# Performance work log

Hardware: AMD Instinct MI355X
Metric: run time of the kernel (lower is better)

## Reference

```python
import jax, jax.numpy as jnp
import numpy as np

NEG_LARGE = -2.0**32 + 1.0


def setup_inputs() -> dict:
    key = jax.random.key(0)
    ks = jax.random.split(key, 8)
    B, L, D = 2048, 200, 64  # D = embedding_dim, features are 2D wide
    H1, H2 = 80, 40
    queries = jax.random.normal(ks[0], (B, 2 * D), dtype=jnp.float32)
    user_behaviors = jax.random.normal(ks[1], (B, L, 2 * D), dtype=jnp.float32)
    masks = jax.random.randint(ks[2], (B, L), 0, 2, dtype=jnp.int32)
    s = 1.0 / np.sqrt(8 * D)
    w1 = jax.random.uniform(ks[3], (8 * D, H1), minval=-s, maxval=s, dtype=jnp.float32)
    b1 = jnp.zeros((H1,), jnp.float32)
    s2 = 1.0 / np.sqrt(H1)
    w2 = jax.random.uniform(ks[4], (H1, H2), minval=-s2, maxval=s2, dtype=jnp.float32)
    b2 = jnp.zeros((H2,), jnp.float32)
    s3 = 1.0 / np.sqrt(H2)
    w3 = jax.random.uniform(ks[5], (H2, 1), minval=-s3, maxval=s3, dtype=jnp.float32)
    b3 = jnp.zeros((1,), jnp.float32)
    return {"queries": queries, "user_behaviors": user_behaviors, "masks": masks,
            "w1": w1, "b1": b1, "w2": w2, "b2": b2, "w3": w3, "b3": b3}


def reference(queries, user_behaviors, masks, w1, b1, w2, b2, w3, b3):
    B, L, twoD = user_behaviors.shape
    q = jnp.broadcast_to(queries[:, None, :], (B, L, twoD))  # (B, L, 2D)
    feats = jnp.concatenate([q, user_behaviors, q - user_behaviors,
                             q * user_behaviors], axis=-1)  # (B, L, 8D)
    h = jax.nn.sigmoid(jnp.einsum('blf,fh->blh', feats, w1) + b1)
    h = jax.nn.sigmoid(jnp.einsum('blh,hk->blk', h, w2) + b2)
    scores = jnp.einsum('blk,ko->blo', h, w3) + b3  # (B, L, 1)
    valid = (masks != 0)[:, :, None]
    scores = jnp.where(valid, scores, NEG_LARGE)
    attn = jax.nn.softmax(scores, axis=1)  # (B, L, 1)
    return jnp.sum(attn * user_behaviors, axis=1)  # (B, 2D)
```

## Files before the change

### kernel.cpp

```cpp
#include <hip/hip_runtime.h>
#include <cstddef>


#define L_   200
#define D2_  128

typedef __attribute__((ext_vector_type(8))) short bf16x8;
typedef __attribute__((ext_vector_type(4))) float f32x4;
typedef __attribute__((ext_vector_type(4))) unsigned int u32x4;

union U8 { u32x4 u; bf16x8 b; };

__device__ __forceinline__ float sigmoidf_(float x) { return 1.0f / (1.0f + __expf(-x)); }

__device__ __forceinline__ unsigned int f2bf_(float x) {
  unsigned int u = __float_as_uint(x);
  return (u + 0x7fffu + ((u >> 16) & 1u)) >> 16;
}
__device__ __forceinline__ unsigned int pk2_(float a, float b) {
  return f2bf_(a) | (f2bf_(b) << 16);
}

extern "C" __global__ void __launch_bounds__(128)
din_setup_kernel(const float* __restrict__ queries,
                 const float* __restrict__ w1,
                 const float* __restrict__ b1,
                 const float* __restrict__ w2,
                 float* __restrict__ qt,
                 float* __restrict__ wbc,
                 float* __restrict__ wd,
                 u32x4* __restrict__ w2a,
                 u32x4* __restrict__ w2b)
{
  const int bb = blockIdx.x;
  const int t  = threadIdx.x;

  if (bb < 8) {
    for (int s = bb * 160 + t; s < bb * 160 + 160; s += 128) {
      int nn = s & 15, kg = (s >> 4) & 3, g = s >> 6;
      int kc = g / 5, nt = g - kc * 5;
      int h = nt * 16 + nn, k0 = kc * 32 + kg * 8;
      #pragma unroll
      for (int j = 0; j < 8; ++j) {
        int k = k0 + j;
        wbc[s * 8 + j] = w1[(128 + k) * 80 + h] - w1[(256 + k) * 80 + h];
        wd [s * 8 + j] = w1[(384 + k) * 80 + h];
      }
    }
  } else if (bb == 8) {
    for (int s = t; s < 384; s += 128) {
      int nn = s & 15, g = s >> 4, nt2 = g >> 3, kg = g & 7;
      int j = nt2 * 16 + nn, k0 = kg * 8;
      u32x4 v = { 0u, 0u, 0u, 0u };
      if (j < 40) {
        float e0 = w2[(k0 + 0) * 40 + j], e1 = w2[(k0 + 1) * 40 + j];
        float e2 = w2[(k0 + 2) * 40 + j], e3 = w2[(k0 + 3) * 40 + j];
        float e4 = w2[(k0 + 4) * 40 + j], e5 = w2[(k0 + 5) * 40 + j];
        float e6 = w2[(k0 + 6) * 40 + j], e7 = w2[(k0 + 7) * 40 + j];
        v = (u32x4){ pk2_(e0, e1), pk2_(e2, e3), pk2_(e4, e5), pk2_(e6, e7) };
      }
      w2a[s] = v;
    }
    for (int s = t; s < 96; s += 128) {
      int nn = s & 15, g = s >> 4, nt2 = g >> 1, kgt = g & 1;
      int j = nt2 * 16 + nn, k0 = 64 + kgt * 8;
      u32x4 v = { 0u, 0u, 0u, 0u };
      if (j < 40) {
        float e0 = w2[(k0 + 0) * 40 + j], e1 = w2[(k0 + 1) * 40 + j];
        float e2 = w2[(k0 + 2) * 40 + j], e3 = w2[(k0 + 3) * 40 + j];
        float e4 = w2[(k0 + 4) * 40 + j], e5 = w2[(k0 + 5) * 40 + j];
        float e6 = w2[(k0 + 6) * 40 + j], e7 = w2[(k0 + 7) * 40 + j];
        v = (u32x4){ pk2_(e0, e1), pk2_(e2, e3), pk2_(e4, e5), pk2_(e6, e7) };
      }
      w2b[s] = v;
    }
  } else {
    const int b = bb - 9;
    __shared__ float qs[128];
    if (t < 128) qs[t] = queries[(size_t)b * D2_ + t];
    __syncthreads();
    if (t < 80) {
      float acc = b1[t];
      #pragma unroll 4
      for (int k = 0; k < 128; ++k)
        acc += qs[k] * (w1[k * 80 + t] + w1[(256 + k) * 80 + t]);
      qt[(size_t)b * 80 + t] = acc;
    }
  }
}

extern "C" __global__ void __launch_bounds__(256, 4)
din_attn_kernel(const float* __restrict__ queries,
                const float* __restrict__ ub,
                const int*   __restrict__ masks,
                const float* __restrict__ b2,
                const float* __restrict__ w3,
                const float* __restrict__ qt,
                const float* __restrict__ wbc,
                const float* __restrict__ wd,
                const u32x4* __restrict__ w2a,
                const u32x4* __restrict__ w2b,
                float* __restrict__ out)
{
  __shared__ __align__(16) char  pool[33280];
  __shared__ __align__(16) float wsum_s[1088];
  __shared__ __align__(16) float qt_s[80];
  __shared__ __align__(16) float b2_s[48];
  __shared__ __align__(16) float w3_s[48];
  __shared__ __align__(16) float scores_s[208];
  __shared__ float red_s[8];

  const int b    = blockIdx.x;
  const int t    = threadIdx.x;
  const int wave = t >> 6;
  const int lane = t & 63;
  const int n16  = lane & 15;
  const int rg   = lane >> 4;

  const float* ubbase = ub + (size_t)b * (L_ * D2_);
  const float* qrow   = queries + (size_t)b * D2_;

  if (t < 80) qt_s[t] = qt[(size_t)b * 80 + t];
  if (t < 48) {
    b2_s[t] = (t < 40) ? b2[t] : 0.0f;
    w3_s[t] = (t < 40) ? w3[t] : 0.0f;
  }

  {
    u32x4* dst = (u32x4*)pool;
    const float4* wbc4 = (const float4*)wbc;
    const float4* wd4  = (const float4*)wd;
    #pragma unroll
    for (int i = 0; i < 5; ++i) {
      int s = i * 256 + t;
      int kg = (s >> 4) & 3, g = s >> 6;
      int kc = g / 5;
      int k0 = kc * 32 + kg * 8;
      float4 c0 = wbc4[2 * s], c1 = wbc4[2 * s + 1];
      float4 d0 = wd4 [2 * s], d1 = wd4 [2 * s + 1];
      float4 q0 = *(const float4*)(qrow + k0);
      float4 q1 = *(const float4*)(qrow + k0 + 4);
      dst[s] = (u32x4){ pk2_(c0.x + q0.x * d0.x, c0.y + q0.y * d0.y),
                        pk2_(c0.z + q0.z * d0.z, c0.w + q0.w * d0.w),
                        pk2_(c1.x + q1.x * d1.x, c1.y + q1.y * d1.y),
                        pk2_(c1.z + q1.z * d1.z, c1.w + q1.w * d1.w) };
    }
  }
  __syncthreads();

  f32x4 acc[4][5];
  #pragma unroll
  for (int i = 0; i < 4; ++i)
    #pragma unroll
    for (int nt = 0; nt < 5; ++nt) acc[i][nt] = (f32x4){0.f, 0.f, 0.f, 0.f};

  const bf16x8* Bf = (const bf16x8*)pool;

  for (int kc = 0; kc < 4; ++kc) {
    bf16x8 bvv[5];
    #pragma unroll
    for (int nt = 0; nt < 5; ++nt) bvv[nt] = Bf[(kc * 5 + nt) * 64 + lane];
    #pragma unroll
    for (int i = 0; i < 4; ++i) {
      int mt = wave + i * 4;
      if (mt < 13) {
        int row = mt * 16 + n16;
        float4 u0 = make_float4(0.f, 0.f, 0.f, 0.f);
        float4 u1 = make_float4(0.f, 0.f, 0.f, 0.f);
        if (row < L_) {
          const float4* src = (const float4*)(ubbase + (size_t)row * D2_ + kc * 32 + rg * 8);
          u0 = src[0]; u1 = src[1];
        }
        U8 av;
        av.u = (u32x4){ pk2_(u0.x, u0.y), pk2_(u0.z, u0.w),
                        pk2_(u1.x, u1.y), pk2_(u1.z, u1.w) };
        #pragma unroll
        for (int nt = 0; nt < 5; ++nt)
          acc[i][nt] = __builtin_amdgcn_mfma_f32_16x16x32_bf16(av.b, bvv[nt], acc[i][nt], 0, 0, 0);
      }
    }
  }
  __syncthreads();

  {
    unsigned short* hv = (unsigned short*)pool;
    #pragma unroll
    for (int i = 0; i < 4; ++i) {
      int mt = wave + i * 4;
      if (mt < 13) {
        #pragma unroll
        for (int nt = 0; nt < 5; ++nt) {
          int h = nt * 16 + n16;
          float qtv = qt_s[h];
          int kg = h >> 3;
          int slotbase = (kg < 8) ? (mt * 8 + kg) : (1664 + mt * 2 + (kg - 8));
          #pragma unroll
          for (int r = 0; r < 4; ++r) {
            float x = acc[i][nt][r] + qtv;
            hv[(slotbase * 16 + rg * 4 + r) * 8 + (h & 7)] =
                (unsigned short)f2bf_(sigmoidf_(x));
          }
        }
      }
    }
  }

  {
    const bf16x8* hvf  = (const bf16x8*)pool;
    const bf16x8* w2af = (const bf16x8*)w2a;
    const bf16x8* w2bf = (const bf16x8*)w2b;
    #pragma unroll
    for (int i = 0; i < 4; ++i) {
      int mt = wave + i * 4;
      if (mt < 13) {
        f32x4 acc2[3];
        #pragma unroll
        for (int n2 = 0; n2 < 3; ++n2) acc2[n2] = (f32x4){0.f, 0.f, 0.f, 0.f};

        #pragma unroll
        for (int ks = 0; ks < 2; ++ks) {
          bf16x8 av = hvf[(mt * 8 + ks * 4 + rg) * 16 + n16];
          #pragma unroll
          for (int n2 = 0; n2 < 3; ++n2) {
            bf16x8 bv = w2af[(n2 * 8 + ks * 4 + rg) * 16 + n16];
            acc2[n2] = __builtin_amdgcn_mfma_f32_16x16x32_bf16(av, bv, acc2[n2], 0, 0, 0);
          }
        }
        {
          bf16x8 av = (bf16x8){0, 0, 0, 0, 0, 0, 0, 0};
          if (lane < 32) av = hvf[(1664 + mt * 2 + rg) * 16 + n16];
          #pragma unroll
          for (int n2 = 0; n2 < 3; ++n2) {
            bf16x8 bv = (bf16x8){0, 0, 0, 0, 0, 0, 0, 0};
            if (lane < 32) bv = w2bf[(n2 * 2 + rg) * 16 + n16];
            acc2[n2] = __builtin_amdgcn_mfma_f32_16x16x32_bf16(av, bv, acc2[n2], 0, 0, 0);
          }
        }

        #pragma unroll
        for (int r = 0; r < 4; ++r) {
          float s = 0.0f;
          #pragma unroll
          for (int n2 = 0; n2 < 3; ++n2) {
            int j = n2 * 16 + n16;
            s += sigmoidf_(acc2[n2][r] + b2_s[j]) * w3_s[j];
          }
          s += __shfl_xor(s, 1, 64);
          s += __shfl_xor(s, 2, 64);
          s += __shfl_xor(s, 4, 64);
          s += __shfl_xor(s, 8, 64);
          int l = mt * 16 + rg * 4 + r;
          if (n16 == 0 && l < L_) scores_s[l] = s;
        }
      }
    }
  }
  __syncthreads();

  float sval = -INFINITY;
  if (t < L_) {
    int mv = masks[(size_t)b * L_ + t];
    sval = mv ? scores_s[t] : -4294967295.0f;
  }
  float m = sval;
  #pragma unroll
  for (int o = 32; o > 0; o >>= 1) m = fmaxf(m, __shfl_xor(m, o, 64));
  if (lane == 0) red_s[wave] = m;
  __syncthreads();
  m = fmaxf(fmaxf(red_s[0], red_s[1]), fmaxf(red_s[2], red_s[3]));
  float e = (t < L_) ? __expf(sval - m) : 0.0f;
  float ssum = e;
  #pragma unroll
  for (int o = 32; o > 0; o >>= 1) ssum += __shfl_xor(ssum, o, 64);
  if (lane == 0) red_s[4 + wave] = ssum;
  __syncthreads();
  ssum = red_s[4] + red_s[5] + red_s[6] + red_s[7];
  float attn = e / ssum;
  __syncthreads();
  if (t < L_) scores_s[t] = attn;
  __syncthreads();

  {
    const float4* ub4base = (const float4*)ubbase;
    int d4 = t & 31;
    int lg = t >> 5;
    float4 o = make_float4(0.f, 0.f, 0.f, 0.f);
    #pragma unroll 5
    for (int l = lg; l < L_; l += 8) {
      float w = scores_s[l];
      float4 v = ub4base[l * 32 + d4];
      o.x += w * v.x; o.y += w * v.y; o.z += w * v.z; o.w += w * v.w;
    }
    *(float4*)(wsum_s + lg * 136 + d4 * 4) = o;
    __syncthreads();
    if (t < 128) {
      float s = 0.0f;
      #pragma unroll
      for (int g = 0; g < 8; ++g) s += wsum_s[g * 136 + t];
      out[(size_t)b * 128 + t] = s;
    }
  }
}

extern "C" void kernel_launch(void* const* d_in, const int* in_sizes, int n_in,
                              void* d_out, int out_size, void* d_ws, size_t ws_size,
                              hipStream_t stream) {
  const float* queries = (const float*)d_in[0];
  const float* ub      = (const float*)d_in[1];
  const int*   masks   = (const int*)d_in[2];
  const float* w1      = (const float*)d_in[3];
  const float* b1      = (const float*)d_in[4];
  const float* w2      = (const float*)d_in[5];
  const float* b2      = (const float*)d_in[6];
  const float* w3      = (const float*)d_in[7];
  float* out = (float*)d_out;

  const int B = in_sizes[0] / D2_;

  char*  ws  = (char*)d_ws;
  float* qt  = (float*)ws;
  float* wbc = (float*)(ws + (size_t)B * 320);
  float* wd  = (float*)(ws + (size_t)B * 320 + 40960);
  u32x4* w2a = (u32x4*)(ws + (size_t)B * 320 + 81920);
  u32x4* w2b = (u32x4*)(ws + (size_t)B * 320 + 88064);

  din_setup_kernel<<<B + 9, 128, 0, stream>>>(queries, w1, b1, w2, qt, wbc, wd, w2a, w2b);
  din_attn_kernel<<<B, 256, 0, stream>>>(queries, ub, masks, b2, w3,
                                         qt, wbc, wd, w2a, w2b, out);
}
```

Measured before the change: 358.1 us.

## Software-pipeline behavior loads in the layer-1 MFMA loop and use hardware bf16 conversion

The layer-1 GEMM is restructured into a fully unrolled, double-buffered sequence. The first behavior-row loads are issued before the shared-memory weight setup, so global latency overlaps that setup and each MFMA step. Out-of-range rows are clamped rather than branched around, so some waves now do wasted MFMA work on padded tiles. Float-to-bf16 packing uses the v_cvt_pk_bf16_f32 instruction, and occupancy is lowered to 3 blocks per SM to make room for the extra registers. The mask load is hoisted to the kernel start, one redundant barrier is removed, and the final weighted-sum loop is fully unrolled.

```diff
diff --git a/kernel.cpp b/kernel.cpp
--- a/kernel.cpp
+++ b/kernel.cpp
@@ -19,6 +19,11 @@
 }
 __device__ __forceinline__ unsigned int pk2_(float a, float b) {
   return f2bf_(a) | (f2bf_(b) << 16);
+}
+__device__ __forceinline__ unsigned int pk2f_(float a, float b) {
+  unsigned int r;
+  asm("v_cvt_pk_bf16_f32 %0, %1, %2" : "=v"(r) : "v"(a), "v"(b));
+  return r;
 }
 
 extern "C" __global__ void __launch_bounds__(128)
@@ -89,7 +94,7 @@
   }
 }
 
-extern "C" __global__ void __launch_bounds__(256, 4)
+extern "C" __global__ void __launch_bounds__(256, 3)
 din_attn_kernel(const float* __restrict__ queries,
                 const float* __restrict__ ub,
                 const int*   __restrict__ masks,
@@ -120,11 +125,65 @@
   const float* ubbase = ub + (size_t)b * (L_ * D2_);
   const float* qrow   = queries + (size_t)b * D2_;
 
+  int mv_early = 1;
+  if (t < L_) mv_early = masks[(size_t)b * L_ + t];
   if (t < 80) qt_s[t] = qt[(size_t)b * 80 + t];
   if (t < 48) {
     b2_s[t] = (t < 40) ? b2[t] : 0.0f;
     w3_s[t] = (t < 40) ? w3[t] : 0.0f;
   }
+
+  const float* pa[4];
+  #pragma unroll
+  for (int i = 0; i < 4; ++i) {
+    int row = (wave + i * 4) * 16 + n16;
+    int rc  = (row < L_) ? row : (L_ - 1);
+    pa[i] = ubbase + (size_t)rc * D2_ + rg * 8;
+  }
+
+  f32x4 acc[4][5];
+  #pragma unroll
+  for (int i = 0; i < 4; ++i)
+    #pragma unroll
+    for (int nt = 0; nt < 5; ++nt) acc[i][nt] = (f32x4){0.f, 0.f, 0.f, 0.f};
+
+  const bf16x8* Bf = (const bf16x8*)pool;
+  bf16x8 bvv[5];
+  float4 A0, A1, B0, B1;
+
+#define LOADP(X0, X1, P) do { \
+    const float4* s_ = (const float4*)(pa[(P) & 3] + ((P) >> 2) * 32); \
+    X0 = s_[0]; X1 = s_[1]; \
+  } while (0)
+
+#define LOADB(KC) do { \
+    bvv[0] = Bf[((KC) * 5 + 0) * 64 + lane]; \
+    bvv[1] = Bf[((KC) * 5 + 1) * 64 + lane]; \
+    bvv[2] = Bf[((KC) * 5 + 2) * 64 + lane]; \
+    bvv[3] = Bf[((KC) * 5 + 3) * 64 + lane]; \
+    bvv[4] = Bf[((KC) * 5 + 4) * 64 + lane]; \
+  } while (0)
+
+#define COMPP(X0, X1, P) do { \
+    U8 av_; \
+    av_.u = (u32x4){ pk2f_(X0.x, X0.y), pk2f_(X0.z, X0.w), \
+                     pk2f_(X1.x, X1.y), pk2f_(X1.z, X1.w) }; \
+    const int i_ = (P) & 3; \
+    acc[i_][0] = __builtin_amdgcn_mfma_f32_16x16x32_bf16(av_.b, bvv[0], acc[i_][0], 0, 0, 0); \
+    acc[i_][1] = __builtin_amdgcn_mfma_f32_16x16x32_bf16(av_.b, bvv[1], acc[i_][1], 0, 0, 0); \
+    acc[i_][2] = __builtin_amdgcn_mfma_f32_16x16x32_bf16(av_.b, bvv[2], acc[i_][2], 0, 0, 0); \
+    acc[i_][3] = __builtin_amdgcn_mfma_f32_16x16x32_bf16(av_.b, bvv[3], acc[i_][3], 0, 0, 0); \
+    acc[i_][4] = __builtin_amdgcn_mfma_f32_16x16x32_bf16(av_.b, bvv[4], acc[i_][4], 0, 0, 0); \
+  } while (0)
+
+#define STEP(X0, X1, P) do { \
+    COMPP(X0, X1, P); \
+    if ((P) + 2 < 16) LOADP(X0, X1, (P) + 2); \
+    if (((P) & 3) == 3 && (P) < 12) LOADB(((P) >> 2) + 1); \
+  } while (0)
+
+  LOADP(A0, A1, 0);
+  LOADP(B0, B1, 1);
 
   {
     u32x4* dst = (u32x4*)pool;
@@ -140,46 +199,24 @@
       float4 d0 = wd4 [2 * s], d1 = wd4 [2 * s + 1];
       float4 q0 = *(const float4*)(qrow + k0);
       float4 q1 = *(const float4*)(qrow + k0 + 4);
-      dst[s] = (u32x4){ pk2_(c0.x + q0.x * d0.x, c0.y + q0.y * d0.y),
-                        pk2_(c0.z + q0.z * d0.z, c0.w + q0.w * d0.w),
-                        pk2_(c1.x + q1.x * d1.x, c1.y + q1.y * d1.y),
-                        pk2_(c1.z + q1.z * d1.z, c1.w + q1.w * d1.w) };
-    }
-  }
-  __syncthreads();
-
-  f32x4 acc[4][5];
-  #pragma unroll
-  for (int i = 0; i < 4; ++i)
-    #pragma unroll
-    for (int nt = 0; nt < 5; ++nt) acc[i][nt] = (f32x4){0.f, 0.f, 0.f, 0.f};
-
-  const bf16x8* Bf = (const bf16x8*)pool;
-
-  for (int kc = 0; kc < 4; ++kc) {
-    bf16x8 bvv[5];
-    #pragma unroll
-    for (int nt = 0; nt < 5; ++nt) bvv[nt] = Bf[(kc * 5 + nt) * 64 + lane];
-    #pragma unroll
-    for (int i = 0; i < 4; ++i) {
-      int mt = wave + i * 4;
-      if (mt < 13) {
-        int row = mt * 16 + n16;
-        float4 u0 = make_float4(0.f, 0.f, 0.f, 0.f);
-        float4 u1 = make_float4(0.f, 0.f, 0.f, 0.f);
-        if (row < L_) {
-          const float4* src = (const float4*)(ubbase + (size_t)row * D2_ + kc * 32 + rg * 8);
-          u0 = src[0]; u1 = src[1];
-        }
-        U8 av;
-        av.u = (u32x4){ pk2_(u0.x, u0.y), pk2_(u0.z, u0.w),
-                        pk2_(u1.x, u1.y), pk2_(u1.z, u1.w) };
-        #pragma unroll
-        for (int nt = 0; nt < 5; ++nt)
-          acc[i][nt] = __builtin_amdgcn_mfma_f32_16x16x32_bf16(av.b, bvv[nt], acc[i][nt], 0, 0, 0);
-      }
-    }
-  }
+      dst[s] = (u32x4){ pk2f_(c0.x + q0.x * d0.x, c0.y + q0.y * d0.y),
+                        pk2f_(c0.z + q0.z * d0.z, c0.w + q0.w * d0.w),
+                        pk2f_(c1.x + q1.x * d1.x, c1.y + q1.y * d1.y),
+                        pk2f_(c1.z + q1.z * d1.z, c1.w + q1.w * d1.w) };
+    }
+  }
+  __syncthreads();
+
+  LOADB(0);
+  STEP(A0, A1, 0);  STEP(B0, B1, 1);
+  STEP(A0, A1, 2);  STEP(B0, B1, 3);
+  STEP(A0, A1, 4);  STEP(B0, B1, 5);
+  STEP(A0, A1, 6);  STEP(B0, B1, 7);
+  STEP(A0, A1, 8);  STEP(B0, B1, 9);
+  STEP(A0, A1, 10); STEP(B0, B1, 11);
+  STEP(A0, A1, 12); STEP(B0, B1, 13);
+  STEP(A0, A1, 14); STEP(B0, B1, 15);
+
   __syncthreads();
 
   {
@@ -258,10 +295,7 @@
   __syncthreads();
 
   float sval = -INFINITY;
-  if (t < L_) {
-    int mv = masks[(size_t)b * L_ + t];
-    sval = mv ? scores_s[t] : -4294967295.0f;
-  }
+  if (t < L_) sval = mv_early ? scores_s[t] : -4294967295.0f;
   float m = sval;
   #pragma unroll
   for (int o = 32; o > 0; o >>= 1) m = fmaxf(m, __shfl_xor(m, o, 64));
@@ -275,9 +309,7 @@
   if (lane == 0) red_s[4 + wave] = ssum;
   __syncthreads();
   ssum = red_s[4] + red_s[5] + red_s[6] + red_s[7];
-  float attn = e / ssum;
-  __syncthreads();
-  if (t < L_) scores_s[t] = attn;
+  if (t < L_) scores_s[t] = e / ssum;
   __syncthreads();
 
   {
@@ -285,7 +317,7 @@
     int d4 = t & 31;
     int lg = t >> 5;
     float4 o = make_float4(0.f, 0.f, 0.f, 0.f);
-    #pragma unroll 5
+    #pragma unroll
     for (int l = lg; l < L_; l += 8) {
       float w = scores_s[l];
       float4 v = ub4base[l * 32 + d4];
@@ -300,6 +332,11 @@
       out[(size_t)b * 128 + t] = s;
     }
   }
+
+#undef LOADP
+#undef LOADB
+#undef COMPP
+#undef STEP
 }
 
 extern "C" void kernel_launch(void* const* d_in, const int* in_sizes, int n_in,
```

After: 382.3 us. +6.8%, slower.

## Prefetch behavior rows into registers and hoist B fragments out of MFMA loop

Applied to the files above, without the earlier changes.

The first-layer MFMA loop now software-pipelines global loads of the user-behavior rows, issuing the first two k-chunks before the weight-prep phase and double-buffering the remaining chunks in registers. All 20 B fragments are loaded from LDS into registers once, up front. Other changes: the packing uses the hardware v_cvt_pk_bf16_f32 instruction, the mask load moves to kernel start, one redundant barrier is dropped, and the weighted-sum loop is fully unrolled. Register pressure rises sharply, which may lower occupancy. Out-of-range rows are clamped to row 199 rather than zeroed, and those rows' results are discarded later.

```diff
diff --git a/kernel.cpp b/kernel.cpp
--- a/kernel.cpp
+++ b/kernel.cpp
@@ -19,6 +19,11 @@
 }
 __device__ __forceinline__ unsigned int pk2_(float a, float b) {
   return f2bf_(a) | (f2bf_(b) << 16);
+}
+__device__ __forceinline__ unsigned int pk2f_(float a, float b) {
+  unsigned int r;
+  asm("v_cvt_pk_bf16_f32 %0, %1, %2" : "=v"(r) : "v"(a), "v"(b));
+  return r;
 }
 
 extern "C" __global__ void __launch_bounds__(128)
@@ -120,11 +125,35 @@
   const float* ubbase = ub + (size_t)b * (L_ * D2_);
   const float* qrow   = queries + (size_t)b * D2_;
 
+  int mv_early = 1;
+  if (t < L_) mv_early = masks[(size_t)b * L_ + t];
   if (t < 80) qt_s[t] = qt[(size_t)b * 80 + t];
   if (t < 48) {
     b2_s[t] = (t < 40) ? b2[t] : 0.0f;
     w3_s[t] = (t < 40) ? w3[t] : 0.0f;
   }
+
+  const float* pa[4];
+  #pragma unroll
+  for (int i = 0; i < 4; ++i) {
+    int row = (wave + i * 4) * 16 + n16;
+    int rc  = (row < L_) ? row : (L_ - 1);
+    pa[i] = ubbase + (size_t)rc * D2_ + rg * 8;
+  }
+
+  float4 ca[4], cb[4], da[4], db[4];
+  #pragma unroll
+  for (int i = 0; i < 4; ++i)
+    if (i < 3 || wave == 0) {
+      const float4* s0 = (const float4*)(pa[i]);
+      ca[i] = s0[0]; cb[i] = s0[1];
+    }
+  #pragma unroll
+  for (int i = 0; i < 4; ++i)
+    if (i < 3 || wave == 0) {
+      const float4* s1 = (const float4*)(pa[i] + 32);
+      da[i] = s1[0]; db[i] = s1[1];
+    }
 
   {
     u32x4* dst = (u32x4*)pool;
@@ -140,12 +169,18 @@
       float4 d0 = wd4 [2 * s], d1 = wd4 [2 * s + 1];
       float4 q0 = *(const float4*)(qrow + k0);
       float4 q1 = *(const float4*)(qrow + k0 + 4);
-      dst[s] = (u32x4){ pk2_(c0.x + q0.x * d0.x, c0.y + q0.y * d0.y),
-                        pk2_(c0.z + q0.z * d0.z, c0.w + q0.w * d0.w),
-                        pk2_(c1.x + q1.x * d1.x, c1.y + q1.y * d1.y),
-                        pk2_(c1.z + q1.z * d1.z, c1.w + q1.w * d1.w) };
-    }
-  }
+      dst[s] = (u32x4){ pk2f_(c0.x + q0.x * d0.x, c0.y + q0.y * d0.y),
+                        pk2f_(c0.z + q0.z * d0.z, c0.w + q0.w * d0.w),
+                        pk2f_(c1.x + q1.x * d1.x, c1.y + q1.y * d1.y),
+                        pk2f_(c1.z + q1.z * d1.z, c1.w + q1.w * d1.w) };
+    }
+  }
+  __syncthreads();
+
+  const bf16x8* Bf = (const bf16x8*)pool;
+  bf16x8 bf[20];
+  #pragma unroll
+  for (int x = 0; x < 20; ++x) bf[x] = Bf[x * 64 + lane];
   __syncthreads();
 
   f32x4 acc[4][5];
@@ -154,33 +189,28 @@
     #pragma unroll
     for (int nt = 0; nt < 5; ++nt) acc[i][nt] = (f32x4){0.f, 0.f, 0.f, 0.f};
 
-  const bf16x8* Bf = (const bf16x8*)pool;
-
+  #pragma unroll
   for (int kc = 0; kc < 4; ++kc) {
-    bf16x8 bvv[5];
-    #pragma unroll
-    for (int nt = 0; nt < 5; ++nt) bvv[nt] = Bf[(kc * 5 + nt) * 64 + lane];
     #pragma unroll
     for (int i = 0; i < 4; ++i) {
-      int mt = wave + i * 4;
-      if (mt < 13) {
-        int row = mt * 16 + n16;
-        float4 u0 = make_float4(0.f, 0.f, 0.f, 0.f);
-        float4 u1 = make_float4(0.f, 0.f, 0.f, 0.f);
-        if (row < L_) {
-          const float4* src = (const float4*)(ubbase + (size_t)row * D2_ + kc * 32 + rg * 8);
-          u0 = src[0]; u1 = src[1];
-        }
+      if (i < 3 || wave == 0) {
+        float4 x0 = (kc & 1) ? da[i] : ca[i];
+        float4 x1 = (kc & 1) ? db[i] : cb[i];
         U8 av;
-        av.u = (u32x4){ pk2_(u0.x, u0.y), pk2_(u0.z, u0.w),
-                        pk2_(u1.x, u1.y), pk2_(u1.z, u1.w) };
+        av.u = (u32x4){ pk2f_(x0.x, x0.y), pk2f_(x0.z, x0.w),
+                        pk2f_(x1.x, x1.y), pk2f_(x1.z, x1.w) };
+        if (kc < 2) {
+          const float4* s2 = (const float4*)(pa[i] + (kc + 2) * 32);
+          if (kc & 1) { da[i] = s2[0]; db[i] = s2[1]; }
+          else        { ca[i] = s2[0]; cb[i] = s2[1]; }
+        }
         #pragma unroll
         for (int nt = 0; nt < 5; ++nt)
-          acc[i][nt] = __builtin_amdgcn_mfma_f32_16x16x32_bf16(av.b, bvv[nt], acc[i][nt], 0, 0, 0);
-      }
-    }
-  }
-  __syncthreads();
+          acc[i][nt] = __builtin_amdgcn_mfma_f32_16x16x32_bf16(av.b, bf[kc * 5 + nt],
+                                                               acc[i][nt], 0, 0, 0);
+      }
+    }
+  }
 
   {
     unsigned short* hv = (unsigned short*)pool;
@@ -258,10 +288,7 @@
   __syncthreads();
 
   float sval = -INFINITY;
-  if (t < L_) {
-    int mv = masks[(size_t)b * L_ + t];
-    sval = mv ? scores_s[t] : -4294967295.0f;
-  }
+  if (t < L_) sval = mv_early ? scores_s[t] : -4294967295.0f;
   float m = sval;
   #pragma unroll
   for (int o = 32; o > 0; o >>= 1) m = fmaxf(m, __shfl_xor(m, o, 64));
@@ -275,9 +302,7 @@
   if (lane == 0) red_s[4 + wave] = ssum;
   __syncthreads();
   ssum = red_s[4] + red_s[5] + red_s[6] + red_s[7];
-  float attn = e / ssum;
-  __syncthreads();
-  if (t < L_) scores_s[t] = attn;
+  if (t < L_) scores_s[t] = e / ssum;
   __syncthreads();
 
   {
@@ -285,7 +310,7 @@
     int d4 = t & 31;
     int lg = t >> 5;
     float4 o = make_float4(0.f, 0.f, 0.f, 0.f);
-    #pragma unroll 5
+    #pragma unroll
     for (int l = lg; l < L_; l += 8) {
       float w = scores_s[l];
       float4 v = ub4base[l * 32 + d4];
```

Result: slower. 481.2 us (+34.4%).

## Split attention kernel into two-block score kernel plus softmax/weighted-sum kernel

Applied to the files above, without the earlier changes.

The fused per-batch attention kernel is split in two. A scores kernel runs two blocks per batch row, each covering part of the 13 row tiles, with per-wave LDS scratch for the hidden layer and smaller shared memory, and writes scores to a workspace buffer. A second kernel then does the masked softmax and the weighted sum over user behaviors. The bf16 packing switches to the hardware v_cvt_pk_bf16_f32 instruction. The aim is more parallelism and occupancy, at the cost of an extra launch, an extra workspace round trip, and reading user_behaviors twice across kernels. The old fused kernel stays as a fallback when the workspace is too small.

```diff
diff --git a/kernel.cpp b/kernel.cpp
--- a/kernel.cpp
+++ b/kernel.cpp
@@ -19,6 +19,11 @@
 }
 __device__ __forceinline__ unsigned int pk2_(float a, float b) {
   return f2bf_(a) | (f2bf_(b) << 16);
+}
+__device__ __forceinline__ unsigned int pk2f_(float a, float b) {
+  unsigned int r;
+  asm("v_cvt_pk_bf16_f32 %0, %1, %2" : "=v"(r) : "v"(a), "v"(b));
+  return r;
 }
 
 extern "C" __global__ void __launch_bounds__(128)
@@ -90,32 +95,34 @@
 }
 
 extern "C" __global__ void __launch_bounds__(256, 4)
-din_attn_kernel(const float* __restrict__ queries,
-                const float* __restrict__ ub,
-                const int*   __restrict__ masks,
-                const float* __restrict__ b2,
-                const float* __restrict__ w3,
-                const float* __restrict__ qt,
-                const float* __restrict__ wbc,
-                const float* __restrict__ wd,
-                const u32x4* __restrict__ w2a,
-                const u32x4* __restrict__ w2b,
-                float* __restrict__ out)
+din_scores_kernel(const float* __restrict__ queries,
+                  const float* __restrict__ ub,
+                  const float* __restrict__ b2,
+                  const float* __restrict__ w3,
+                  const float* __restrict__ qt,
+                  const float* __restrict__ wbc,
+                  const float* __restrict__ wd,
+                  const u32x4* __restrict__ w2a,
+                  const u32x4* __restrict__ w2b,
+                  float* __restrict__ scores_ws)
 {
-  __shared__ __align__(16) char  pool[33280];
-  __shared__ __align__(16) float wsum_s[1088];
+  __shared__ __align__(16) char  pool[20480];
+  __shared__ __align__(16) char  scratch[10240];
   __shared__ __align__(16) float qt_s[80];
   __shared__ __align__(16) float b2_s[48];
   __shared__ __align__(16) float w3_s[48];
-  __shared__ __align__(16) float scores_s[208];
-  __shared__ float red_s[8];
-
-  const int b    = blockIdx.x;
-  const int t    = threadIdx.x;
-  const int wave = t >> 6;
-  const int lane = t & 63;
-  const int n16  = lane & 15;
-  const int rg   = lane >> 4;
+
+  const int bc    = blockIdx.x;
+  const int b     = bc >> 1;
+  const int chunk = bc & 1;
+  const int t     = threadIdx.x;
+  const int wave  = t >> 6;
+  const int lane  = t & 63;
+  const int n16   = lane & 15;
+  const int rg    = lane >> 4;
+
+  const int st  = chunk ? (wave < 2 ? 7 + wave * 2 : 9 + wave) : wave * 2;
+  const int cnt = chunk ? (wave < 2 ? 2 : 1) : (wave < 3 ? 2 : 1);
 
   const float* ubbase = ub + (size_t)b * (L_ * D2_);
   const float* qrow   = queries + (size_t)b * D2_;
@@ -140,10 +147,232 @@
       float4 d0 = wd4 [2 * s], d1 = wd4 [2 * s + 1];
       float4 q0 = *(const float4*)(qrow + k0);
       float4 q1 = *(const float4*)(qrow + k0 + 4);
-      dst[s] = (u32x4){ pk2_(c0.x + q0.x * d0.x, c0.y + q0.y * d0.y),
-                        pk2_(c0.z + q0.z * d0.z, c0.w + q0.w * d0.w),
-                        pk2_(c1.x + q1.x * d1.x, c1.y + q1.y * d1.y),
-                        pk2_(c1.z + q1.z * d1.z, c1.w + q1.w * d1.w) };
+      dst[s] = (u32x4){ pk2f_(c0.x + q0.x * d0.x, c0.y + q0.y * d0.y),
+                        pk2f_(c0.z + q0.z * d0.z, c0.w + q0.w * d0.w),
+                        pk2f_(c1.x + q1.x * d1.x, c1.y + q1.y * d1.y),
+                        pk2f_(c1.z + q1.z * d1.z, c1.w + q1.w * d1.w) };
+    }
+  }
+  __syncthreads();
+
+  const float* pa[2];
+  #pragma unroll
+  for (int i = 0; i < 2; ++i) {
+    int row = (st + i) * 16 + n16;
+    int rc  = (row < L_) ? row : (L_ - 1);
+    pa[i] = ubbase + (size_t)rc * D2_ + rg * 8;
+  }
+
+  f32x4 acc[2][5];
+  #pragma unroll
+  for (int i = 0; i < 2; ++i)
+    #pragma unroll
+    for (int nt = 0; nt < 5; ++nt) acc[i][nt] = (f32x4){0.f, 0.f, 0.f, 0.f};
+
+  const bf16x8* Bf = (const bf16x8*)pool;
+  for (int kc = 0; kc < 4; ++kc) {
+    U8 av[2];
+    #pragma unroll
+    for (int i = 0; i < 2; ++i) {
+      if (i < cnt) {
+        const float4* src = (const float4*)(pa[i] + kc * 32);
+        float4 u0 = src[0], u1 = src[1];
+        av[i].u = (u32x4){ pk2f_(u0.x, u0.y), pk2f_(u0.z, u0.w),
+                           pk2f_(u1.x, u1.y), pk2f_(u1.z, u1.w) };
+      }
+    }
+    #pragma unroll
+    for (int nt = 0; nt < 5; ++nt) {
+      bf16x8 bv = Bf[(kc * 5 + nt) * 64 + lane];
+      #pragma unroll
+      for (int i = 0; i < 2; ++i)
+        if (i < cnt)
+          acc[i][nt] = __builtin_amdgcn_mfma_f32_16x16x32_bf16(av[i].b, bv, acc[i][nt], 0, 0, 0);
+    }
+  }
+
+  {
+    unsigned short* hv  = (unsigned short*)(scratch + wave * 2560);
+    const bf16x8*   hvf = (const bf16x8*)(scratch + wave * 2560);
+    const bf16x8*   w2af = (const bf16x8*)w2a;
+    const bf16x8*   w2bf = (const bf16x8*)w2b;
+
+    for (int i = 0; i < 2; ++i) {
+      if (i < cnt) {
+        const int mt = st + i;
+
+        #pragma unroll
+        for (int nt = 0; nt < 5; ++nt) {
+          int h  = nt * 16 + n16;
+          int kg = h >> 3;
+          float qtv = qt_s[h];
+          #pragma unroll
+          for (int r = 0; r < 4; ++r) {
+            float x = acc[i][nt][r] + qtv;
+            hv[(kg * 16 + rg * 4 + r) * 8 + (h & 7)] = (unsigned short)f2bf_(sigmoidf_(x));
+          }
+        }
+
+        f32x4 acc2[3];
+        #pragma unroll
+        for (int n2 = 0; n2 < 3; ++n2) acc2[n2] = (f32x4){0.f, 0.f, 0.f, 0.f};
+
+        #pragma unroll
+        for (int ks = 0; ks < 2; ++ks) {
+          bf16x8 av = hvf[(ks * 4 + rg) * 16 + n16];
+          #pragma unroll
+          for (int n2 = 0; n2 < 3; ++n2) {
+            bf16x8 bv = w2af[(n2 * 8 + ks * 4 + rg) * 16 + n16];
+            acc2[n2] = __builtin_amdgcn_mfma_f32_16x16x32_bf16(av, bv, acc2[n2], 0, 0, 0);
+          }
+        }
+        {
+          bf16x8 av = (bf16x8){0, 0, 0, 0, 0, 0, 0, 0};
+          if (lane < 32) av = hvf[(8 + rg) * 16 + n16];
+          #pragma unroll
+          for (int n2 = 0; n2 < 3; ++n2) {
+            bf16x8 bv = (bf16x8){0, 0, 0, 0, 0, 0, 0, 0};
+            if (lane < 32) bv = w2bf[(n2 * 2 + rg) * 16 + n16];
+            acc2[n2] = __builtin_amdgcn_mfma_f32_16x16x32_bf16(av, bv, acc2[n2], 0, 0, 0);
+          }
+        }
+
+        #pragma unroll
+        for (int r = 0; r < 4; ++r) {
+          float s = 0.0f;
+          #pragma unroll
+          for (int n2 = 0; n2 < 3; ++n2) {
+            int j = n2 * 16 + n16;
+            s += sigmoidf_(acc2[n2][r] + b2_s[j]) * w3_s[j];
+          }
+          s += __shfl_xor(s, 1, 64);
+          s += __shfl_xor(s, 2, 64);
+          s += __shfl_xor(s, 4, 64);
+          s += __shfl_xor(s, 8, 64);
+          int l = mt * 16 + rg * 4 + r;
+          if (n16 == 0 && l < L_) scores_ws[(size_t)b * L_ + l] = s;
+        }
+      }
+    }
+  }
+}
+
+extern "C" __global__ void __launch_bounds__(256, 4)
+din_softmax_wsum_kernel(const float* __restrict__ ub,
+                        const int*   __restrict__ masks,
+                        const float* __restrict__ scores_ws,
+                        float* __restrict__ out)
+{
+  __shared__ __align__(16) float scores_s[208];
+  __shared__ __align__(16) float wsum_s[1088];
+  __shared__ float red_s[8];
+
+  const int b    = blockIdx.x;
+  const int t    = threadIdx.x;
+  const int wave = t >> 6;
+  const int lane = t & 63;
+
+  const float* ubbase = ub + (size_t)b * (L_ * D2_);
+
+  float sval = -INFINITY;
+  if (t < L_) {
+    int   mv = masks[(size_t)b * L_ + t];
+    float sc = scores_ws[(size_t)b * L_ + t];
+    sval = mv ? sc : -4294967295.0f;
+  }
+  float m = sval;
+  #pragma unroll
+  for (int o = 32; o > 0; o >>= 1) m = fmaxf(m, __shfl_xor(m, o, 64));
+  if (lane == 0) red_s[wave] = m;
+  __syncthreads();
+  m = fmaxf(fmaxf(red_s[0], red_s[1]), fmaxf(red_s[2], red_s[3]));
+  float e = (t < L_) ? __expf(sval - m) : 0.0f;
+  float ssum = e;
+  #pragma unroll
+  for (int o = 32; o > 0; o >>= 1) ssum += __shfl_xor(ssum, o, 64);
+  if (lane == 0) red_s[4 + wave] = ssum;
+  __syncthreads();
+  ssum = red_s[4] + red_s[5] + red_s[6] + red_s[7];
+  if (t < L_) scores_s[t] = e / ssum;
+  __syncthreads();
+
+  {
+    const float4* ub4base = (const float4*)ubbase;
+    int d4 = t & 31;
+    int lg = t >> 5;
+    float4 o = make_float4(0.f, 0.f, 0.f, 0.f);
+    #pragma unroll
+    for (int l = lg; l < L_; l += 8) {
+      float w = scores_s[l];
+      float4 v = ub4base[l * 32 + d4];
+      o.x += w * v.x; o.y += w * v.y; o.z += w * v.z; o.w += w * v.w;
+    }
+    *(float4*)(wsum_s + lg * 136 + d4 * 4) = o;
+    __syncthreads();
+    if (t < 128) {
+      float s = 0.0f;
+      #pragma unroll
+      for (int g = 0; g < 8; ++g) s += wsum_s[g * 136 + t];
+      out[(size_t)b * 128 + t] = s;
+    }
+  }
+}
+
+extern "C" __global__ void __launch_bounds__(256, 4)
+din_attn_fallback(const float* __restrict__ queries,
+                  const float* __restrict__ ub,
+                  const int*   __restrict__ masks,
+                  const float* __restrict__ b2,
+                  const float* __restrict__ w3,
+                  const float* __restrict__ qt,
+                  const float* __restrict__ wbc,
+                  const float* __restrict__ wd,
+                  const u32x4* __restrict__ w2a,
+                  const u32x4* __restrict__ w2b,
+                  float* __restrict__ out)
+{
+  __shared__ __align__(16) char  pool[33280];
+  __shared__ __align__(16) float wsum_s[1088];
+  __shared__ __align__(16) float qt_s[80];
+  __shared__ __align__(16) float b2_s[48];
+  __shared__ __align__(16) float w3_s[48];
+  __shared__ __align__(16) float scores_s[208];
+  __shared__ float red_s[8];
+
+  const int b    = blockIdx.x;
+  const int t    = threadIdx.x;
+  const int wave = t >> 6;
+  const int lane = t & 63;
+  const int n16  = lane & 15;
+  const int rg   = lane >> 4;
+
+  const float* ubbase = ub + (size_t)b * (L_ * D2_);
+  const float* qrow   = queries + (size_t)b * D2_;
+
+  if (t < 80) qt_s[t] = qt[(size_t)b * 80 + t];
+  if (t < 48) {
+    b2_s[t] = (t < 40) ? b2[t] : 0.0f;
+    w3_s[t] = (t < 40) ? w3[t] : 0.0f;
+  }
+
+  {
+    u32x4* dst = (u32x4*)pool;
+    const float4* wbc4 = (const float4*)wbc;
+    const float4* wd4  = (const float4*)wd;
+    #pragma unroll
+    for (int i = 0; i < 5; ++i) {
+      int s = i * 256 + t;
+      int kg = (s >> 4) & 3, g = s >> 6;
+      int kc = g / 5;
+      int k0 = kc * 32 + kg * 8;
+      float4 c0 = wbc4[2 * s], c1 = wbc4[2 * s + 1];
+      float4 d0 = wd4 [2 * s], d1 = wd4 [2 * s + 1];
+      float4 q0 = *(const float4*)(qrow + k0);
+      float4 q1 = *(const float4*)(qrow + k0 + 4);
+      dst[s] = (u32x4){ pk2f_(c0.x + q0.x * d0.x, c0.y + q0.y * d0.y),
+                        pk2f_(c0.z + q0.z * d0.z, c0.w + q0.w * d0.w),
+                        pk2f_(c1.x + q1.x * d1.x, c1.y + q1.y * d1.y),
+                        pk2f_(c1.z + q1.z * d1.z, c1.w + q1.w * d1.w) };
     }
   }
   __syncthreads();
@@ -155,7 +384,6 @@
     for (int nt = 0; nt < 5; ++nt) acc[i][nt] = (f32x4){0.f, 0.f, 0.f, 0.f};
 
   const bf16x8* Bf = (const bf16x8*)pool;
-
   for (int kc = 0; kc < 4; ++kc) {
     bf16x8 bvv[5];
     #pragma unroll
@@ -172,8 +400,8 @@
           u0 = src[0]; u1 = src[1];
         }
         U8 av;
-        av.u = (u32x4){ pk2_(u0.x, u0.y), pk2_(u0.z, u0.w),
-                        pk2_(u1.x, u1.y), pk2_(u1.z, u1.w) };
+        av.u = (u32x4){ pk2f_(u0.x, u0.y), pk2f_(u0.z, u0.w),
+                        pk2f_(u1.x, u1.y), pk2f_(u1.z, u1.w) };
         #pragma unroll
         for (int nt = 0; nt < 5; ++nt)
           acc[i][nt] = __builtin_amdgcn_mfma_f32_16x16x32_bf16(av.b, bvv[nt], acc[i][nt], 0, 0, 0);
@@ -216,7 +444,6 @@
         f32x4 acc2[3];
         #pragma unroll
         for (int n2 = 0; n2 < 3; ++n2) acc2[n2] = (f32x4){0.f, 0.f, 0.f, 0.f};
-
         #pragma unroll
         for (int ks = 0; ks < 2; ++ks) {
           bf16x8 av = hvf[(mt * 8 + ks * 4 + rg) * 16 + n16];
@@ -236,7 +463,6 @@
             acc2[n2] = __builtin_amdgcn_mfma_f32_16x16x32_bf16(av, bv, acc2[n2], 0, 0, 0);
           }
         }
-
         #pragma unroll
         for (int r = 0; r < 4; ++r) {
           float s = 0.0f;
@@ -275,9 +501,7 @@
   if (lane == 0) red_s[4 + wave] = ssum;
   __syncthreads();
   ssum = red_s[4] + red_s[5] + red_s[6] + red_s[7];
-  float attn = e / ssum;
-  __syncthreads();
-  if (t < L_) scores_s[t] = attn;
+  if (t < L_) scores_s[t] = e / ssum;
   __syncthreads();
 
   {
@@ -285,7 +509,7 @@
     int d4 = t & 31;
     int lg = t >> 5;
     float4 o = make_float4(0.f, 0.f, 0.f, 0.f);
-    #pragma unroll 5
+    #pragma unroll
     for (int l = lg; l < L_; l += 8) {
       float w = scores_s[l];
       float4 v = ub4base[l * 32 + d4];
@@ -323,8 +547,18 @@
   float* wd  = (float*)(ws + (size_t)B * 320 + 40960);
   u32x4* w2a = (u32x4*)(ws + (size_t)B * 320 + 81920);
   u32x4* w2b = (u32x4*)(ws + (size_t)B * 320 + 88064);
+  size_t sc_off = (size_t)B * 320 + 90112;
+  float* scores = (float*)(ws + sc_off);
+  size_t need = sc_off + (size_t)B * L_ * 4;
 
   din_setup_kernel<<<B + 9, 128, 0, stream>>>(queries, w1, b1, w2, qt, wbc, wd, w2a, w2b);
-  din_attn_kernel<<<B, 256, 0, stream>>>(queries, ub, masks, b2, w3,
-                                         qt, wbc, wd, w2a, w2b, out);
-}
+
+  if (ws_size >= need) {
+    din_scores_kernel<<<2 * B, 256, 0, stream>>>(queries, ub, b2, w3,
+                                                 qt, wbc, wd, w2a, w2b, scores);
+    din_softmax_wsum_kernel<<<B, 256, 0, stream>>>(ub, masks, scores, out);
+  } else {
+    din_attn_fallback<<<B, 256, 0, stream>>>(queries, ub, masks, b2, w3,
+                                             qt, wbc, wd, w2a, w2b, out);
+  }
+}
```

Result: slower. 375.0 us (+4.7%).
